# Kernel optimization log

Measured on AMD Instinct MI355X. Metric: run time of the kernel, lower is better.

## Reference

```python
import jax, jax.numpy as jnp
import numpy as np
from jax.scipy.linalg import expm

B, T, N_IN, N_HID, N_OUT = 8192, 2048, 2, 10, 10


def setup_inputs() -> dict:
    key = jax.random.key(0)
    k0, k1, k2, k3, k4 = jax.random.split(key, 5)
    inputs = jax.random.normal(k0, (B, T, N_IN), dtype=jnp.float32)
    # skew-symmetric seed for the orthogonal recurrent kernel (expm parametrization)
    A = jax.random.normal(k1, (N_HID, N_HID), dtype=jnp.float32) * 0.1
    # input_kernel: nn.Linear(n_inputs, n_hidden, bias=False) -> weight [H, D_in]
    W_in = jax.random.normal(k2, (N_HID, N_IN), dtype=jnp.float32) / np.sqrt(N_IN)
    # modrelu bias, initialized uniform(-0.01, 0.01) as in exprnn
    b_mod = jax.random.uniform(k3, (N_HID,), jnp.float32, -0.01, 0.01)
    # final nn.Linear(n_hidden, n_outputs)
    lin_W = jax.random.normal(k4, (N_OUT, N_HID), dtype=jnp.float32) / np.sqrt(N_HID)
    lin_b = jnp.zeros((N_OUT,), jnp.float32)
    return {"inputs": inputs, "A": A, "W_in": W_in, "b_mod": b_mod,
            "lin_W": lin_W, "lin_b": lin_b}


def _modrelu(z, b):
    # modrelu(z) = sign(z) * relu(|z| + b)
    return jnp.sign(z) * jax.nn.relu(jnp.abs(z) + b)


def reference(inputs, A, W_in, b_mod, lin_W, lin_b):
    # Orthogonal recurrent matrix: Bmat = expm(skew(A)), skew from strict upper triangle
    A_tri = jnp.triu(A, k=1)
    Bmat = expm(A_tri - A_tri.T)  # [H, H], orthogonal
    # Precompute input projections for all timesteps: [B, T, H]
    x_proj = jnp.einsum('btd,hd->bth', inputs, W_in)
    h0 = jnp.zeros((inputs.shape[0], W_in.shape[0]), dtype=inputs.dtype)

    def step(h, x_t):
        h_new = _modrelu(x_t + h @ Bmat, b_mod)
        return h_new, None

    hT, _ = jax.lax.scan(step, h0, jnp.swapaxes(x_proj, 0, 1))  # scan over time
    out = hT @ lin_W.T + lin_b  # [B, n_outputs]
    return out
```

## Files before the change

### kernel.cpp

```cpp
#include <hip/hip_runtime.h>
#include <hip/hip_bf16.h>

#define H 10
#define T_LEN 2048
#define BATCH 8192
#define GPW 6

__global__ void expm_kernel(const float* __restrict__ A, float* __restrict__ Bout) {
    __shared__ double S[H][H];
    __shared__ double P[H][H];
    __shared__ double E[H][H];
    const int tid = threadIdx.x;
    const int i = tid / H, j = tid % H;
    if (tid < H * H) {
        double a = 0.0;
        if (i < j) a = (double)A[i * H + j];
        else if (i > j) a = -(double)A[j * H + i];
        a *= (1.0 / 256.0);
        S[i][j] = a;
        P[i][j] = a;
        E[i][j] = (i == j ? 1.0 : 0.0) + a;
    }
    __syncthreads();
    for (int k = 2; k <= 16; ++k) {
        double acc = 0.0;
        if (tid < H * H) {
            for (int m = 0; m < H; ++m) acc += P[i][m] * S[m][j];
            acc *= (1.0 / (double)k);
        }
        __syncthreads();
        if (tid < H * H) { P[i][j] = acc; E[i][j] += acc; }
        __syncthreads();
    }
    for (int rr = 0; rr < 8; ++rr) {
        double acc = 0.0;
        if (tid < H * H) {
            for (int m = 0; m < H; ++m) acc += E[i][m] * E[m][j];
        }
        __syncthreads();
        if (tid < H * H) E[i][j] = acc;
        __syncthreads();
    }
    if (tid < H * H) Bout[i * H + j] = (float)E[i][j];
}

__global__ __launch_bounds__(64)
void rnn_kernel(const float* __restrict__ x,
                const float* __restrict__ Bm_g,
                const float* __restrict__ Win,
                const float* __restrict__ bmod,
                const float* __restrict__ lW,
                const float* __restrict__ lb,
                float* __restrict__ out) {
    __shared__ float hsh[(GPW + 1) * 12];

    const int lane = threadIdx.x;
    const int g = lane / 10;
    const int r = lane - g * 10;
    const int bb_raw = blockIdx.x * GPW + g;
    const bool active = (g < GPW) && (bb_raw < BATCH);
    const int bb = active ? bb_raw : 0;
    float* const hb = &hsh[g * 12];

    float Bcol[H];
#pragma unroll
    for (int i = 0; i < H; ++i) Bcol[i] = Bm_g[i * H + r];
    const float w0 = Win[r * 2 + 0];
    const float w1 = Win[r * 2 + 1];
    const float bm = bmod[r];
    float h = 0.0f;

    const float4* __restrict__ xp4 =
        (const float4*)(x + (size_t)bb * (T_LEN * 2));

    float4 buf0 = xp4[0], buf1 = xp4[1], buf2 = xp4[2], buf3 = xp4[3];

    for (int t0 = 0; t0 < T_LEN; t0 += 8) {
        const float4 c0 = buf0, c1 = buf1, c2 = buf2, c3 = buf3;
        if (t0 + 8 < T_LEN) {
            const int base = (t0 + 8) >> 1;
            buf0 = xp4[base + 0];
            buf1 = xp4[base + 1];
            buf2 = xp4[base + 2];
            buf3 = xp4[base + 3];
        }
        float xs[16];
        xs[0] = c0.x; xs[1] = c0.y; xs[2]  = c0.z; xs[3]  = c0.w;
        xs[4] = c1.x; xs[5] = c1.y; xs[6]  = c1.z; xs[7]  = c1.w;
        xs[8] = c2.x; xs[9] = c2.y; xs[10] = c2.z; xs[11] = c2.w;
        xs[12] = c3.x; xs[13] = c3.y; xs[14] = c3.z; xs[15] = c3.w;

#pragma unroll
        for (int u = 0; u < 8; ++u) {
            const float x0 = xs[2 * u], x1 = xs[2 * u + 1];
            hb[r] = h;
            __syncthreads();
            const float4 ha = *(const float4*)(hb);
            const float4 hbv = *(const float4*)(hb + 4);
            const float2 hc = *(const float2*)(hb + 8);

            float acc = fmaf(x1, w1, x0 * w0);
            float cA = ha.x * Bcol[0];
            float cB = ha.y * Bcol[1];
            cA = fmaf(ha.z,  Bcol[2], cA);
            cB = fmaf(ha.w,  Bcol[3], cB);
            cA = fmaf(hbv.x, Bcol[4], cA);
            cB = fmaf(hbv.y, Bcol[5], cB);
            cA = fmaf(hbv.z, Bcol[6], cA);
            cB = fmaf(hbv.w, Bcol[7], cB);
            cA = fmaf(hc.x,  Bcol[8], cA);
            cB = fmaf(hc.y,  Bcol[9], cB);
            acc = acc + cA + cB;

            const float rr = fmaxf(fabsf(acc) + bm, 0.0f);
            h = __builtin_copysignf(rr, acc);
        }
    }

    hb[r] = h;
    __syncthreads();
    const float4 ha = *(const float4*)(hb);
    const float4 hbv = *(const float4*)(hb + 4);
    const float2 hc = *(const float2*)(hb + 8);
    if (active) {
        float acc = lb[r];
        acc = fmaf(ha.x,  lW[r * H + 0], acc);
        acc = fmaf(ha.y,  lW[r * H + 1], acc);
        acc = fmaf(ha.z,  lW[r * H + 2], acc);
        acc = fmaf(ha.w,  lW[r * H + 3], acc);
        acc = fmaf(hbv.x, lW[r * H + 4], acc);
        acc = fmaf(hbv.y, lW[r * H + 5], acc);
        acc = fmaf(hbv.z, lW[r * H + 6], acc);
        acc = fmaf(hbv.w, lW[r * H + 7], acc);
        acc = fmaf(hc.x,  lW[r * H + 8], acc);
        acc = fmaf(hc.y,  lW[r * H + 9], acc);
        out[(size_t)bb * H + r] = acc;
    }
}

extern "C" void kernel_launch(void* const* d_in, const int* in_sizes, int n_in,
                              void* d_out, int out_size, void* d_ws, size_t ws_size,
                              hipStream_t stream) {
    const float* inputs = (const float*)d_in[0];
    const float* A      = (const float*)d_in[1];
    const float* W_in   = (const float*)d_in[2];
    const float* b_mod  = (const float*)d_in[3];
    const float* lin_W  = (const float*)d_in[4];
    const float* lin_b  = (const float*)d_in[5];
    float* out = (float*)d_out;
    float* Bmat = (float*)d_ws;

    expm_kernel<<<1, 128, 0, stream>>>(A, Bmat);
    const int nblocks = (BATCH + GPW - 1) / GPW;
    rnn_kernel<<<nblocks, 64, 0, stream>>>(inputs, Bmat, W_in, b_mod,
                                           lin_W, lin_b, out);
}
```

Measured before the change: 360.2 us.

## Replace LDS hidden-state exchange with DPP row rotations and packed FMA

```diff
diff --git a/kernel.cpp b/kernel.cpp
--- a/kernel.cpp
+++ b/kernel.cpp
@@ -1,10 +1,18 @@
 #include <hip/hip_runtime.h>
-#include <hip/hip_bf16.h>
 
 #define H 10
 #define T_LEN 2048
 #define BATCH 8192
-#define GPW 6
+
+typedef float v2f __attribute__((ext_vector_type(2)));
+
+__device__ __forceinline__ v2f vdup(float s) { v2f r; r.x = s; r.y = s; return r; }
+__device__ __forceinline__ v2f vfma2(v2f a, v2f b, v2f c) {
+    return __builtin_elementwise_fma(a, b, c);
+}
+
+#define ROR2K(x, K) __int_as_float(__builtin_amdgcn_update_dpp(                  \
+    0, __float_as_int(x), 0x120 + 2 * (K), 0xF, 0xF, true))
 
 __global__ void expm_kernel(const float* __restrict__ A, float* __restrict__ Bout) {
     __shared__ double S[H][H];
@@ -46,95 +54,111 @@
 
 __global__ __launch_bounds__(64)
 void rnn_kernel(const float* __restrict__ x,
-                const float* __restrict__ Bm_g,
+                const float* __restrict__ Bm,
                 const float* __restrict__ Win,
                 const float* __restrict__ bmod,
                 const float* __restrict__ lW,
                 const float* __restrict__ lb,
                 float* __restrict__ out) {
-    __shared__ float hsh[(GPW + 1) * 12];
+    const int lane = threadIdx.x;
+    const int l16  = lane & 15;
+    const int row  = lane >> 4;
+    const int par  = l16 & 1;
+    const int q    = l16 >> 1;
+    const int bb   = blockIdx.x * 8 + row * 2 + par;
+    const int o0   = 2 * q, o1 = o0 + 1;
 
-    const int lane = threadIdx.x;
-    const int g = lane / 10;
-    const int r = lane - g * 10;
-    const int bb_raw = blockIdx.x * GPW + g;
-    const bool active = (g < GPW) && (bb_raw < BATCH);
-    const int bb = active ? bb_raw : 0;
-    float* const hb = &hsh[g * 12];
+    v2f Br0[8], Br1[8];
+#pragma unroll
+    for (int k = 0; k < 8; ++k) {
+        const int m = (q - k) & 7;
+        const int j0 = 2 * m, j1 = j0 + 1;
+        v2f b0 = vdup(0.f), b1 = vdup(0.f);
+        if (o0 < H) {
+            if (j0 < H) b0.x = Bm[j0 * H + o0];
+            if (j1 < H) b1.x = Bm[j1 * H + o0];
+        }
+        if (o1 < H) {
+            if (j0 < H) b0.y = Bm[j0 * H + o1];
+            if (j1 < H) b1.y = Bm[j1 * H + o1];
+        }
+        Br0[k] = b0; Br1[k] = b1;
+    }
+    v2f w0v = vdup(0.f), w1v = vdup(0.f), bmv = vdup(0.f);
+    if (o0 < H) { w0v.x = Win[o0 * 2]; w1v.x = Win[o0 * 2 + 1]; bmv.x = bmod[o0]; }
+    if (o1 < H) { w0v.y = Win[o1 * 2]; w1v.y = Win[o1 * 2 + 1]; bmv.y = bmod[o1]; }
 
-    float Bcol[H];
+    float hx = 0.f, hy = 0.f;
+
+    const float4* __restrict__ xp4 = (const float4*)(x + (size_t)bb * (T_LEN * 2));
+    float4 buf[8];
 #pragma unroll
-    for (int i = 0; i < H; ++i) Bcol[i] = Bm_g[i * H + r];
-    const float w0 = Win[r * 2 + 0];
-    const float w1 = Win[r * 2 + 1];
-    const float bm = bmod[r];
-    float h = 0.0f;
+    for (int i = 0; i < 8; ++i) buf[i] = xp4[i];
 
-    const float4* __restrict__ xp4 =
-        (const float4*)(x + (size_t)bb * (T_LEN * 2));
-
-    float4 buf0 = xp4[0], buf1 = xp4[1], buf2 = xp4[2], buf3 = xp4[3];
-
-    for (int t0 = 0; t0 < T_LEN; t0 += 8) {
-        const float4 c0 = buf0, c1 = buf1, c2 = buf2, c3 = buf3;
-        if (t0 + 8 < T_LEN) {
-            const int base = (t0 + 8) >> 1;
-            buf0 = xp4[base + 0];
-            buf1 = xp4[base + 1];
-            buf2 = xp4[base + 2];
-            buf3 = xp4[base + 3];
+    for (int t0 = 0; t0 < T_LEN; t0 += 16) {
+        float4 c[8];
+#pragma unroll
+        for (int i = 0; i < 8; ++i) c[i] = buf[i];
+        if (t0 + 16 < T_LEN) {
+            const int base = (t0 + 16) >> 1;
+#pragma unroll
+            for (int i = 0; i < 8; ++i) buf[i] = xp4[base + i];
         }
-        float xs[16];
-        xs[0] = c0.x; xs[1] = c0.y; xs[2]  = c0.z; xs[3]  = c0.w;
-        xs[4] = c1.x; xs[5] = c1.y; xs[6]  = c1.z; xs[7]  = c1.w;
-        xs[8] = c2.x; xs[9] = c2.y; xs[10] = c2.z; xs[11] = c2.w;
-        xs[12] = c3.x; xs[13] = c3.y; xs[14] = c3.z; xs[15] = c3.w;
+        float xs[32];
+#pragma unroll
+        for (int i = 0; i < 8; ++i) {
+            xs[4 * i + 0] = c[i].x; xs[4 * i + 1] = c[i].y;
+            xs[4 * i + 2] = c[i].z; xs[4 * i + 3] = c[i].w;
+        }
 
 #pragma unroll
-        for (int u = 0; u < 8; ++u) {
+        for (int u = 0; u < 16; ++u) {
             const float x0 = xs[2 * u], x1 = xs[2 * u + 1];
-            hb[r] = h;
-            __syncthreads();
-            const float4 ha = *(const float4*)(hb);
-            const float4 hbv = *(const float4*)(hb + 4);
-            const float2 hc = *(const float2*)(hb + 8);
-
-            float acc = fmaf(x1, w1, x0 * w0);
-            float cA = ha.x * Bcol[0];
-            float cB = ha.y * Bcol[1];
-            cA = fmaf(ha.z,  Bcol[2], cA);
-            cB = fmaf(ha.w,  Bcol[3], cB);
-            cA = fmaf(hbv.x, Bcol[4], cA);
-            cB = fmaf(hbv.y, Bcol[5], cB);
-            cA = fmaf(hbv.z, Bcol[6], cA);
-            cB = fmaf(hbv.w, Bcol[7], cB);
-            cA = fmaf(hc.x,  Bcol[8], cA);
-            cB = fmaf(hc.y,  Bcol[9], cB);
-            acc = acc + cA + cB;
-
-            const float rr = fmaxf(fabsf(acc) + bm, 0.0f);
-            h = __builtin_copysignf(rr, acc);
+            v2f accA = vfma2(vdup(x1), w1v, vdup(x0) * w0v);
+            v2f accB = vdup(hx) * Br0[0];
+            accA = vfma2(vdup(hy), Br1[0], accA);
+#define DOTK(K) { const float ex_ = ROR2K(hx, K); const float ey_ = ROR2K(hy, K); \
+                  accB = vfma2(vdup(ex_), Br0[K], accB);                          \
+                  accA = vfma2(vdup(ey_), Br1[K], accA); }
+            DOTK(1) DOTK(2) DOTK(3) DOTK(4) DOTK(5) DOTK(6) DOTK(7)
+#undef DOTK
+            const v2f s = accA + accB;
+            const float rx = fmaxf(fabsf(s.x) + bmv.x, 0.f);
+            const float ry = fmaxf(fabsf(s.y) + bmv.y, 0.f);
+            hx = __builtin_copysignf(rx, s.x);
+            hy = __builtin_copysignf(ry, s.y);
         }
     }
 
-    hb[r] = h;
-    __syncthreads();
-    const float4 ha = *(const float4*)(hb);
-    const float4 hbv = *(const float4*)(hb + 4);
-    const float2 hc = *(const float2*)(hb + 8);
-    if (active) {
-        float acc = lb[r];
-        acc = fmaf(ha.x,  lW[r * H + 0], acc);
-        acc = fmaf(ha.y,  lW[r * H + 1], acc);
-        acc = fmaf(ha.z,  lW[r * H + 2], acc);
-        acc = fmaf(ha.w,  lW[r * H + 3], acc);
-        acc = fmaf(hbv.x, lW[r * H + 4], acc);
-        acc = fmaf(hbv.y, lW[r * H + 5], acc);
-        acc = fmaf(hbv.z, lW[r * H + 6], acc);
-        acc = fmaf(hbv.w, lW[r * H + 7], acc);
-        acc = fmaf(hc.x,  lW[r * H + 8], acc);
-        acc = fmaf(hc.y,  lW[r * H + 9], acc);
-        out[(size_t)bb * H + r] = acc;
+    v2f L0[8], L1[8];
+#pragma unroll
+    for (int k = 0; k < 8; ++k) {
+        const int m = (q - k) & 7;
+        const int j0 = 2 * m, j1 = j0 + 1;
+        v2f a0 = vdup(0.f), a1 = vdup(0.f);
+        if (o0 < H) {
+            if (j0 < H) a0.x = lW[o0 * H + j0];
+            if (j1 < H) a1.x = lW[o0 * H + j1];
+        }
+        if (o1 < H) {
+            if (j0 < H) a0.y = lW[o1 * H + j0];
+            if (j1 < H) a1.y = lW[o1 * H + j1];
+        }
+        L0[k] = a0; L1[k] = a1;
+    }
+    v2f accO = vdup(0.f);
+    if (o0 < H) accO.x = lb[o0];
+    if (o1 < H) accO.y = lb[o1];
+    accO = vfma2(vdup(hx), L0[0], accO);
+    accO = vfma2(vdup(hy), L1[0], accO);
+#define OUTK(K) { const float ex_ = ROR2K(hx, K); const float ey_ = ROR2K(hy, K); \
+                  accO = vfma2(vdup(ex_), L0[K], accO);                           \
+                  accO = vfma2(vdup(ey_), L1[K], accO); }
+    OUTK(1) OUTK(2) OUTK(3) OUTK(4) OUTK(5) OUTK(6) OUTK(7)
+#undef OUTK
+    if (o0 < H) {
+        float2 st; st.x = accO.x; st.y = accO.y;
+        *reinterpret_cast<float2*>(out + (size_t)bb * H + o0) = st;
     }
 }
 
@@ -151,7 +175,6 @@
     float* Bmat = (float*)d_ws;
 
     expm_kernel<<<1, 128, 0, stream>>>(A, Bmat);
-    const int nblocks = (BATCH + GPW - 1) / GPW;
-    rnn_kernel<<<nblocks, 64, 0, stream>>>(inputs, Bmat, W_in, b_mod,
-                                           lin_W, lin_b, out);
+    rnn_kernel<<<BATCH / 8, 64, 0, stream>>>(inputs, Bmat, W_in, b_mod,
+                                             lin_W, lin_b, out);
 }
```

Result: faster. 343.2 us (-4.7%).
